# Kernel optimization log

Measured on AMD Instinct MI355X. Metric: run time of the kernel, lower is better.

The kernel has to match this reference:

```python
import jax, jax.numpy as jnp
import numpy as np

N_NODES = 100000
N_EDGES = 1600000
N_GRAPHS = 512
IN_C, HID, OUT_C = 128, 128, 64


def gcn_conv(x, W, b, src, dst, num_nodes):
    # PyG GCNConv: add self-loops, symmetric normalization D^-1/2 (A+I) D^-1/2, then linear.
    h = x @ W  # [N, F_out]
    deg = jnp.ones((num_nodes,), h.dtype).at[dst].add(jnp.ones((src.shape[0],), h.dtype))  # +1 for self-loop
    dinv = jax.lax.rsqrt(deg)
    norm = dinv[src] * dinv[dst]  # [E]
    agg = jnp.zeros_like(h).at[dst].add(h[src] * norm[:, None])
    agg = agg + h * (dinv * dinv)[:, None]  # self-loop contribution
    return agg + b


def global_mean_pool(x, batch, num_graphs):
    s = jax.ops.segment_sum(x, batch, num_segments=num_graphs)
    cnt = jax.ops.segment_sum(jnp.ones((x.shape[0],), x.dtype), batch, num_segments=num_graphs)
    return s / jnp.maximum(cnt, 1.0)[:, None]


def setup_inputs() -> dict:
    key = jax.random.key(0)
    ks = jax.random.split(key, 16)
    glorot = lambda k, i, o: jax.random.normal(k, (i, o), jnp.float32) * (2.0 / (i + o)) ** 0.5
    inp = {
        "x": jax.random.normal(ks[0], (N_NODES, IN_C), jnp.float32),
        "edge_index": jax.random.randint(ks[1], (2, N_EDGES), 0, N_NODES, jnp.int64 if jax.config.jax_enable_x64 else jnp.int32),
        "batch": jnp.sort(jax.random.randint(ks[2], (N_NODES,), 0, N_GRAPHS)),
        "W1": glorot(ks[3], IN_C, HID), "b1": jnp.zeros((HID,), jnp.float32),
        "W2": glorot(ks[4], HID, HID), "b2": jnp.zeros((HID,), jnp.float32),
        "W3": glorot(ks[5], HID, HID), "b3": jnp.zeros((HID,), jnp.float32),
        "Wf1": glorot(ks[6], HID, HID * 4), "bf1": jnp.zeros((HID * 4,), jnp.float32),
        "Wf2": glorot(ks[7], HID * 4, HID * 2), "bf2": jnp.zeros((HID * 2,), jnp.float32),
        "Wf3": glorot(ks[8], HID * 2, HID), "bf3": jnp.zeros((HID,), jnp.float32),
        "Wf4": glorot(ks[9], HID, OUT_C), "bf4": jnp.zeros((OUT_C,), jnp.float32),
    }
    return inp


def reference(x, edge_index, batch, W1, b1, W2, b2, W3, b3,
              Wf1, bf1, Wf2, bf2, Wf3, bf3, Wf4, bf4):
    src, dst = edge_index[0], edge_index[1]
    h = jax.nn.relu(gcn_conv(x, W1, b1, src, dst, N_NODES))
    h = jax.nn.relu(gcn_conv(h, W2, b2, src, dst, N_NODES))
    h = gcn_conv(h, W3, b3, src, dst, N_NODES)
    f = global_mean_pool(h, batch, N_GRAPHS)  # [G, HID]
    z = jax.nn.relu(f @ Wf1 + bf1)
    z = jax.nn.relu(z @ Wf2 + bf2)
    z = jax.nn.relu(z @ Wf3 + bf3)
    z = z @ Wf4 + bf4
    return (f, z)
```

## Files before the change

### kernel.cpp

```cpp
#include <hip/hip_runtime.h>
#include <hip/hip_bf16.h>

#define NN 100000
#define NE 1600000
#define NG 512
#define HID 128
#define PPART 391
#define EPB 4096

typedef __attribute__((ext_vector_type(8))) short short8;
typedef __attribute__((ext_vector_type(4))) float floatx4;

__device__ inline ushort f2bf(float f) {
  uint u = __float_as_uint(f);
  u += 0x7fff + ((u >> 16) & 1);
  return (ushort)(u >> 16);
}
__device__ inline uint pack2(float lo, float hi) {
  return (uint)f2bf(lo) | ((uint)f2bf(hi) << 16);
}
__device__ inline float bflo(uint u) { return __uint_as_float(u << 16); }
__device__ inline float bfhi(uint u) { return __uint_as_float(u & 0xffff0000u); }

__global__ __launch_bounds__(256) void k_hist(const int* __restrict__ dst,
                                              int* __restrict__ phist) {
  __shared__ int h[PPART];
  int t = threadIdx.x;
  for (int i = t; i < PPART; i += 256) h[i] = 0;
  __syncthreads();
  int e0 = blockIdx.x * EPB;
#pragma unroll
  for (int l = 0; l < 16; ++l) {
    int e = e0 + l * 256 + t;
    if (e < NE) atomicAdd(&h[dst[e] >> 8], 1);
  }
  __syncthreads();
  for (int i = t; i < PPART; i += 256)
    if (h[i]) atomicAdd(&phist[i], h[i]);
}

__global__ __launch_bounds__(512) void k_pscan(const int* __restrict__ phist,
                                               int* __restrict__ pbase) {
  __shared__ int ws[8];
  int t = threadIdx.x, lane = t & 63, wid = t >> 6;
  int v = (t < PPART) ? phist[t] : 0;
  int iv = v;
  for (int o = 1; o < 64; o <<= 1) {
    int n = __shfl_up(iv, o, 64);
    if (lane >= o) iv += n;
  }
  if (lane == 63) ws[wid] = iv;
  __syncthreads();
  int add = 0;
#pragma unroll
  for (int w = 0; w < 8; ++w) add += (w < wid) ? ws[w] : 0;
  if (t < PPART) pbase[t] = iv - v + add;
  if (t == 0) {
    int tot = 0;
#pragma unroll
    for (int w = 0; w < 8; ++w) tot += ws[w];
    pbase[PPART] = tot;
  }
}

__global__ void k_pinit(const int* __restrict__ pbase, int* __restrict__ pcur) {
  int p = blockIdx.x * 256 + threadIdx.x;
  if (p < PPART) pcur[p] = pbase[p];
}

__global__ __launch_bounds__(256) void k_part(const int* __restrict__ src,
                                              const int* __restrict__ dst,
                                              int* __restrict__ pcur,
                                              uint* __restrict__ pedge) {
  __shared__ int hist[PPART];
  __shared__ int base[PPART];
  int t = threadIdx.x;
  for (int i = t; i < PPART; i += 256) hist[i] = 0;
  __syncthreads();
  int e0 = blockIdx.x * EPB;
  int d_[16];
#pragma unroll
  for (int l = 0; l < 16; ++l) {
    int e = e0 + l * 256 + t;
    if (e < NE) {
      int d = dst[e];
      d_[l] = d;
      atomicAdd(&hist[d >> 8], 1);
    } else {
      d_[l] = -1;
    }
  }
  __syncthreads();
  for (int i = t; i < PPART; i += 256) {
    int h = hist[i];
    base[i] = h ? atomicAdd(&pcur[i], h) : 0;
  }
  __syncthreads();
#pragma unroll
  for (int l = 0; l < 16; ++l) {
    int e = e0 + l * 256 + t;
    if (e < NE) {
      int d = d_[l];
      int s = src[e];
      int pos = atomicAdd(&base[d >> 8], 1);
      pedge[pos] = (uint)s | ((uint)(d & 255) << 24);
    }
  }
}

__global__ __launch_bounds__(256) void k_bucket2(const int* __restrict__ pbase,
                                                 const uint* __restrict__ pedge,
                                                 int* __restrict__ srcs,
                                                 int* __restrict__ offsets,
                                                 float* __restrict__ dinv) {
  __shared__ int cnt_s[256];
  __shared__ int cur[256];
  __shared__ int ws[4];
  int p = blockIdx.x;
  int n0 = p << 8;
  int t = threadIdx.x;
  int lim = NN - n0; if (lim > 256) lim = 256;
  int s = pbase[p], e = pbase[p + 1];
  cnt_s[t] = 0;
  __syncthreads();
  for (int i = s + t; i < e; i += 256) atomicAdd(&cnt_s[pedge[i] >> 24], 1);
  __syncthreads();
  int v = cnt_s[t];
  int lane = t & 63, wid = t >> 6;
  int iv = v;
  for (int o = 1; o < 64; o <<= 1) {
    int n = __shfl_up(iv, o, 64);
    if (lane >= o) iv += n;
  }
  if (lane == 63) ws[wid] = iv;
  __syncthreads();
  int add = 0;
#pragma unroll
  for (int w = 0; w < 4; ++w) add += (w < wid) ? ws[w] : 0;
  int excl = iv - v + add;
  if (t < lim) {
    int o = s + excl;
    offsets[n0 + t] = o;
    cur[t] = o;
    dinv[n0 + t] = 1.0f / sqrtf((float)(v + 1));
  }
  if (p == PPART - 1 && t == 0) offsets[NN] = NE;
  __syncthreads();
  for (int i = s + t; i < e; i += 256) {
    uint pv = pedge[i];
    int pos = atomicAdd(&cur[pv >> 24], 1);
    srcs[pos] = (int)(pv & 0xFFFFFFu);
  }
}

__global__ void k_cast(const float4* __restrict__ x, uint2* __restrict__ xb, int n4) {
  int i = blockIdx.x * 256 + threadIdx.x;
  if (i < n4) {
    float4 v = x[i];
    uint2 o;
    o.x = pack2(v.x, v.y);
    o.y = pack2(v.z, v.w);
    xb[i] = o;
  }
}

__global__ __launch_bounds__(128) void k_prepW(const float* __restrict__ W,
                                               ushort* __restrict__ wt) {
  int c = blockIdx.x;
  int r = threadIdx.x;
  float v = W[r * 128 + c];
  wt[c * 128 + (((r >> 3) ^ (c & 15)) << 3) + (r & 7)] = f2bf(v);
}

__global__ __launch_bounds__(256) void k_gemm(const ushort* __restrict__ Xb,
                                              const ushort* __restrict__ wt,
                                              ushort* __restrict__ Hb) {
  __shared__ ushort sW[128 * 128];
  int t = threadIdx.x;
#pragma unroll
  for (int l = 0; l < 8; ++l) {
    int idx = t + l * 256;
    ((uint4*)sW)[idx] = ((const uint4*)wt)[idx];
  }
  __syncthreads();
  int wid = t >> 6, lane = t & 63;
  int row0 = blockIdx.x * 64 + wid * 16;
  int arow = row0 + (lane & 15);
  if (arow >= NN) arow = NN - 1;
  const ushort* aptr = Xb + (size_t)arow * 128 + ((lane >> 4) * 8);
  floatx4 acc[8];
#pragma unroll
  for (int n = 0; n < 8; ++n) acc[n] = (floatx4)(0.f);
#pragma unroll
  for (int kb = 0; kb < 4; ++kb) {
    short8 a = *(const short8*)(aptr + kb * 32);
    int kslot = kb * 4 + (lane >> 4);
#pragma unroll
    for (int n = 0; n < 8; ++n) {
      int col = n * 16 + (lane & 15);
      const ushort* bp = sW + col * 128 + ((kslot ^ (col & 15)) << 3);
      short8 b = *(const short8*)bp;
      acc[n] = __builtin_amdgcn_mfma_f32_16x16x32_bf16(a, b, acc[n], 0, 0, 0);
    }
  }
  int srow_base = row0 + (lane >> 4) * 4;
#pragma unroll
  for (int r = 0; r < 4; ++r) {
    int grow = srow_base + r;
    if (grow < NN) {
      ushort* out = Hb + (size_t)grow * 128 + (lane & 15);
#pragma unroll
      for (int n = 0; n < 8; ++n) out[n * 16] = f2bf(acc[n][r]);
    }
  }
}

__global__ __launch_bounds__(256) void k_agg(const ushort* __restrict__ H,
                                             const float* __restrict__ bias,
                                             const float* __restrict__ dinv,
                                             const int* __restrict__ offsets,
                                             const int* __restrict__ srcs,
                                             ushort* __restrict__ Hout, int do_relu) {
  int node = blockIdx.x * 16 + (threadIdx.x >> 4);
  if (node >= NN) return;
  int c8 = threadIdx.x & 15;
  float di = dinv[node];
  int s = offsets[node], e = offsets[node + 1];
  float acc[8];
#pragma unroll
  for (int j = 0; j < 8; ++j) acc[j] = 0.f;
  for (int i = s; i < e; i += 8) {
    int sx[8];
    float dx[8];
    uint4 vx[8];
#pragma unroll
    for (int u = 0; u < 8; ++u) {
      int idx = i + u;
      bool vld = idx < e;
      sx[u] = srcs[vld ? idx : s];
      dx[u] = vld ? 1.0f : 0.0f;
    }
#pragma unroll
    for (int u = 0; u < 8; ++u) dx[u] *= dinv[sx[u]];
#pragma unroll
    for (int u = 0; u < 8; ++u) vx[u] = *((const uint4*)(H + (size_t)sx[u] * 128) + c8);
#pragma unroll
    for (int u = 0; u < 8; ++u) {
      acc[0] += bflo(vx[u].x) * dx[u];
      acc[1] += bfhi(vx[u].x) * dx[u];
      acc[2] += bflo(vx[u].y) * dx[u];
      acc[3] += bfhi(vx[u].y) * dx[u];
      acc[4] += bflo(vx[u].z) * dx[u];
      acc[5] += bfhi(vx[u].z) * dx[u];
      acc[6] += bflo(vx[u].w) * dx[u];
      acc[7] += bfhi(vx[u].w) * dx[u];
    }
  }
  uint4 hv = *((const uint4*)(H + (size_t)node * 128) + c8);
  float hb[8] = {bflo(hv.x), bfhi(hv.x), bflo(hv.y), bfhi(hv.y),
                 bflo(hv.z), bfhi(hv.z), bflo(hv.w), bfhi(hv.w)};
  float dii = di * di;
  const float* bp = bias + c8 * 8;
  float r[8];
#pragma unroll
  for (int j = 0; j < 8; ++j) {
    float vv = acc[j] * di + hb[j] * dii + bp[j];
    if (do_relu) vv = fmaxf(vv, 0.f);
    r[j] = vv;
  }
  uint4 o;
  o.x = pack2(r[0], r[1]);
  o.y = pack2(r[2], r[3]);
  o.z = pack2(r[4], r[5]);
  o.w = pack2(r[6], r[7]);
  *((uint4*)(Hout + (size_t)node * 128) + c8) = o;
}

__device__ inline int lower_bound(const int* a, int n, int v) {
  int lo = 0, hi = n;
  while (lo < hi) {
    int m = (lo + hi) >> 1;
    if (a[m] < v) lo = m + 1; else hi = m;
  }
  return lo;
}

__global__ __launch_bounds__(128) void k_pool(const ushort* __restrict__ H,
                                              const int* __restrict__ batch,
                                              float* __restrict__ f) {
  int g = blockIdx.x;
  int c = threadIdx.x;
  int s = lower_bound(batch, NN, g);
  int e = lower_bound(batch, NN, g + 1);
  float acc = 0.f;
#pragma unroll 4
  for (int i = s; i < e; ++i)
    acc += __uint_as_float(((uint)H[(size_t)i * 128 + c]) << 16);
  f[g * 128 + c] = acc / fmaxf((float)(e - s), 1.0f);
}

__global__ __launch_bounds__(256) void k_mgemm(const float* __restrict__ X,
                                               const float* __restrict__ W,
                                               const float* __restrict__ bias,
                                               float* __restrict__ Y,
                                               int M, int K, int N, int do_relu) {
  __shared__ float sA[32][32];
  __shared__ float sB[32][64];
  int t = threadIdx.x;
  int tn = t & 15, tm = t >> 4;
  int m0 = blockIdx.y * 32;
  int n0 = blockIdx.x * 64;
  float acc[2][4];
#pragma unroll
  for (int i = 0; i < 2; ++i)
#pragma unroll
    for (int j = 0; j < 4; ++j) acc[i][j] = 0.f;

  for (int kb = 0; kb < K; kb += 32) {
    {
      int r = t >> 3, kq = t & 7;
      float4 v = *(const float4*)(X + (size_t)(m0 + r) * K + kb + kq * 4);
      sA[kq * 4 + 0][r] = v.x;
      sA[kq * 4 + 1][r] = v.y;
      sA[kq * 4 + 2][r] = v.z;
      sA[kq * 4 + 3][r] = v.w;
    }
#pragma unroll
    for (int l = 0; l < 2; ++l) {
      int idx = t * 2 + l;
      int kr = idx >> 4, nq = idx & 15;
      *(float4*)&sB[kr][nq * 4] = *(const float4*)(W + (size_t)(kb + kr) * N + n0 + nq * 4);
    }
    __syncthreads();
#pragma unroll
    for (int k = 0; k < 32; ++k) {
      float a[2], b[4];
      a[0] = sA[k][tm * 2];
      a[1] = sA[k][tm * 2 + 1];
      *(float4*)b = *(float4*)&sB[k][tn * 4];
#pragma unroll
      for (int i = 0; i < 2; ++i)
#pragma unroll
        for (int j = 0; j < 4; ++j) acc[i][j] += a[i] * b[j];
    }
    __syncthreads();
  }
  float4 bv = *(const float4*)(bias + n0 + tn * 4);
#pragma unroll
  for (int i = 0; i < 2; ++i) {
    float4 o;
    o.x = acc[i][0] + bv.x;
    o.y = acc[i][1] + bv.y;
    o.z = acc[i][2] + bv.z;
    o.w = acc[i][3] + bv.w;
    if (do_relu) {
      o.x = fmaxf(o.x, 0.f);
      o.y = fmaxf(o.y, 0.f);
      o.z = fmaxf(o.z, 0.f);
      o.w = fmaxf(o.w, 0.f);
    }
    *(float4*)(Y + (size_t)(m0 + tm * 2 + i) * N + n0 + tn * 4) = o;
  }
}

extern "C" void kernel_launch(void* const* d_in, const int* in_sizes, int n_in,
                              void* d_out, int out_size, void* d_ws, size_t ws_size,
                              hipStream_t stream) {
  const float* x    = (const float*)d_in[0];
  const int* ei     = (const int*)d_in[1];
  const int* batch  = (const int*)d_in[2];
  const float* W1   = (const float*)d_in[3];  const float* b1  = (const float*)d_in[4];
  const float* W2   = (const float*)d_in[5];  const float* b2  = (const float*)d_in[6];
  const float* W3   = (const float*)d_in[7];  const float* b3  = (const float*)d_in[8];
  const float* Wf1  = (const float*)d_in[9];  const float* bf1 = (const float*)d_in[10];
  const float* Wf2  = (const float*)d_in[11]; const float* bf2 = (const float*)d_in[12];
  const float* Wf3  = (const float*)d_in[13]; const float* bf3 = (const float*)d_in[14];
  const float* Wf4  = (const float*)d_in[15]; const float* bf4 = (const float*)d_in[16];
  const int* src = ei;
  const int* dst = ei + NE;

  char* ws = (char*)d_ws;
  size_t off = 0;
  auto alloc = [&](size_t bytes) {
    void* p = ws + off;
    off += (bytes + 255) & ~(size_t)255;
    return p;
  };
  ushort* B0     = (ushort*)alloc((size_t)NN * 128 * 2);
  ushort* B1     = (ushort*)alloc((size_t)NN * 128 * 2);
  ushort* B2     = (ushort*)alloc((size_t)NN * 128 * 2);
  float* dinv    = (float*)alloc((size_t)NN * 4);
  int*   offsets = (int*)alloc((size_t)(NN + 1) * 4);
  int*   srcs    = (int*)alloc((size_t)NE * 4);
  uint*  pedge   = (uint*)alloc((size_t)NE * 4);
  int*   phist   = (int*)alloc((size_t)PPART * 4);
  int*   pbase   = (int*)alloc((size_t)(PPART + 1) * 4);
  int*   pcur    = (int*)alloc((size_t)PPART * 4);
  ushort* wt1    = (ushort*)alloc(128 * 128 * 2);
  ushort* wt2    = (ushort*)alloc(128 * 128 * 2);
  ushort* wt3    = (ushort*)alloc(128 * 128 * 2);
  float* t1      = (float*)alloc((size_t)NG * 512 * 4);
  float* t2      = (float*)alloc((size_t)NG * 256 * 4);
  float* t3      = (float*)alloc((size_t)NG * 128 * 4);

  float* f_out = (float*)d_out;
  float* z_out = (float*)d_out + NG * HID;

  hipMemsetAsync(phist, 0, (size_t)PPART * 4, stream);
  k_hist<<<(NE + EPB - 1) / EPB, 256, 0, stream>>>(dst, phist);
  k_pscan<<<1, 512, 0, stream>>>(phist, pbase);
  k_pinit<<<(PPART + 255) / 256, 256, 0, stream>>>(pbase, pcur);
  k_part<<<(NE + EPB - 1) / EPB, 256, 0, stream>>>(src, dst, pcur, pedge);
  k_bucket2<<<PPART, 256, 0, stream>>>(pbase, pedge, srcs, offsets, dinv);

  k_prepW<<<128, 128, 0, stream>>>(W1, wt1);
  k_prepW<<<128, 128, 0, stream>>>(W2, wt2);
  k_prepW<<<128, 128, 0, stream>>>(W3, wt3);
  k_cast<<<(NN * 128 / 4 + 255) / 256, 256, 0, stream>>>((const float4*)x, (uint2*)B0, NN * 128 / 4);

  int gemm_grid = (NN + 63) / 64;
  int agg_grid = (NN + 15) / 16;

  k_gemm<<<gemm_grid, 256, 0, stream>>>(B0, wt1, B1);
  k_agg<<<agg_grid, 256, 0, stream>>>(B1, b1, dinv, offsets, srcs, B2, 1);
  k_gemm<<<gemm_grid, 256, 0, stream>>>(B2, wt2, B1);
  k_agg<<<agg_grid, 256, 0, stream>>>(B1, b2, dinv, offsets, srcs, B0, 1);
  k_gemm<<<gemm_grid, 256, 0, stream>>>(B0, wt3, B1);
  k_agg<<<agg_grid, 256, 0, stream>>>(B1, b3, dinv, offsets, srcs, B2, 0);

  k_pool<<<NG, 128, 0, stream>>>(B2, batch, f_out);

  k_mgemm<<<dim3(8, 16), 256, 0, stream>>>(f_out, Wf1, bf1, t1, NG, 128, 512, 1);
  k_mgemm<<<dim3(4, 16), 256, 0, stream>>>(t1, Wf2, bf2, t2, NG, 512, 256, 1);
  k_mgemm<<<dim3(2, 16), 256, 0, stream>>>(t2, Wf3, bf3, t3, NG, 256, 128, 1);
  k_mgemm<<<dim3(1, 16), 256, 0, stream>>>(t3, Wf4, bf4, z_out, NG, 128, 64, 0);
}
```

Before: 381.4 us.

## Precompute per-edge (src, dinv) metadata and load it cooperatively via shuffles in aggregation

Adds a kernel that packs each CSR edge's source index and the source's dinv into an int2 array, so aggregation no longer does a dependent gather of dinv per edge. In k_agg, the 16 lanes serving a node each load one edge's metadata and broadcast it with wave shuffles, replacing eight redundant per-lane loads of srcs and dinv. It also folds the pcur initialisation into the scan kernel, removing one launch. In exchange it adds an NE-sized buffer, an extra pass over the edges, and loop padding to multiples of 16 edges.

After: 387.3 us. Within noise of the previous version (+1.5%).

```diff
diff --git a/kernel.cpp b/kernel.cpp
--- a/kernel.cpp
+++ b/kernel.cpp
@@ -40,7 +40,8 @@
 }
 
 __global__ __launch_bounds__(512) void k_pscan(const int* __restrict__ phist,
-                                               int* __restrict__ pbase) {
+                                               int* __restrict__ pbase,
+                                               int* __restrict__ pcur) {
   __shared__ int ws[8];
   int t = threadIdx.x, lane = t & 63, wid = t >> 6;
   int v = (t < PPART) ? phist[t] : 0;
@@ -54,18 +55,17 @@
   int add = 0;
 #pragma unroll
   for (int w = 0; w < 8; ++w) add += (w < wid) ? ws[w] : 0;
-  if (t < PPART) pbase[t] = iv - v + add;
+  if (t < PPART) {
+    int b = iv - v + add;
+    pbase[t] = b;
+    pcur[t] = b;
+  }
   if (t == 0) {
     int tot = 0;
 #pragma unroll
     for (int w = 0; w < 8; ++w) tot += ws[w];
     pbase[PPART] = tot;
   }
-}
-
-__global__ void k_pinit(const int* __restrict__ pbase, int* __restrict__ pcur) {
-  int p = blockIdx.x * 256 + threadIdx.x;
-  if (p < PPART) pcur[p] = pbase[p];
 }
 
 __global__ __launch_bounds__(256) void k_part(const int* __restrict__ src,
@@ -153,6 +153,19 @@
   }
 }
 
+__global__ void k_emeta(const int* __restrict__ srcs,
+                        const float* __restrict__ dinv,
+                        int2* __restrict__ emeta) {
+  int i = blockIdx.x * 256 + threadIdx.x;
+  if (i < NE) {
+    int s = srcs[i];
+    int2 m;
+    m.x = s;
+    m.y = __float_as_int(dinv[s]);
+    emeta[i] = m;
+  }
+}
+
 __global__ void k_cast(const float4* __restrict__ x, uint2* __restrict__ xb, int n4) {
   int i = blockIdx.x * 256 + threadIdx.x;
   if (i < n4) {
@@ -219,41 +232,49 @@
                                              const float* __restrict__ bias,
                                              const float* __restrict__ dinv,
                                              const int* __restrict__ offsets,
-                                             const int* __restrict__ srcs,
+                                             const int2* __restrict__ emeta,
                                              ushort* __restrict__ Hout, int do_relu) {
   int node = blockIdx.x * 16 + (threadIdx.x >> 4);
   if (node >= NN) return;
-  int c8 = threadIdx.x & 15;
+  int lane = threadIdx.x & 63;
+  int c8 = lane & 15;
+  int gbase = lane & 48;
   float di = dinv[node];
   int s = offsets[node], e = offsets[node + 1];
   float acc[8];
 #pragma unroll
   for (int j = 0; j < 8; ++j) acc[j] = 0.f;
-  for (int i = s; i < e; i += 8) {
-    int sx[8];
-    float dx[8];
-    uint4 vx[8];
-#pragma unroll
-    for (int u = 0; u < 8; ++u) {
-      int idx = i + u;
-      bool vld = idx < e;
-      sx[u] = srcs[vld ? idx : s];
-      dx[u] = vld ? 1.0f : 0.0f;
-    }
-#pragma unroll
-    for (int u = 0; u < 8; ++u) dx[u] *= dinv[sx[u]];
-#pragma unroll
-    for (int u = 0; u < 8; ++u) vx[u] = *((const uint4*)(H + (size_t)sx[u] * 128) + c8);
-#pragma unroll
-    for (int u = 0; u < 8; ++u) {
-      acc[0] += bflo(vx[u].x) * dx[u];
-      acc[1] += bfhi(vx[u].x) * dx[u];
-      acc[2] += bflo(vx[u].y) * dx[u];
-      acc[3] += bfhi(vx[u].y) * dx[u];
-      acc[4] += bflo(vx[u].z) * dx[u];
-      acc[5] += bfhi(vx[u].z) * dx[u];
-      acc[6] += bflo(vx[u].w) * dx[u];
-      acc[7] += bfhi(vx[u].w) * dx[u];
+  for (int i = s; i < e; i += 16) {
+    int idx = i + c8;
+    bool vld = idx < e;
+    int2 m = emeta[vld ? idx : s];
+    int msrc = m.x;
+    float mw = vld ? __int_as_float(m.y) : 0.0f;
+#pragma unroll
+    for (int half = 0; half < 2; ++half) {
+      int sxu[8];
+      float wu[8];
+#pragma unroll
+      for (int u = 0; u < 8; ++u) {
+        int sl = gbase + half * 8 + u;
+        sxu[u] = __shfl(msrc, sl, 64);
+        wu[u] = __shfl(mw, sl, 64);
+      }
+      uint4 vx[8];
+#pragma unroll
+      for (int u = 0; u < 8; ++u)
+        vx[u] = *((const uint4*)(H + (size_t)sxu[u] * 128) + c8);
+#pragma unroll
+      for (int u = 0; u < 8; ++u) {
+        acc[0] += bflo(vx[u].x) * wu[u];
+        acc[1] += bfhi(vx[u].x) * wu[u];
+        acc[2] += bflo(vx[u].y) * wu[u];
+        acc[3] += bfhi(vx[u].y) * wu[u];
+        acc[4] += bflo(vx[u].z) * wu[u];
+        acc[5] += bfhi(vx[u].z) * wu[u];
+        acc[6] += bflo(vx[u].w) * wu[u];
+        acc[7] += bfhi(vx[u].w) * wu[u];
+      }
     }
   }
   uint4 hv = *((const uint4*)(H + (size_t)node * 128) + c8);
@@ -393,6 +414,7 @@
   int*   offsets = (int*)alloc((size_t)(NN + 1) * 4);
   int*   srcs    = (int*)alloc((size_t)NE * 4);
   uint*  pedge   = (uint*)alloc((size_t)NE * 4);
+  int2*  emeta   = (int2*)alloc((size_t)NE * 8);
   int*   phist   = (int*)alloc((size_t)PPART * 4);
   int*   pbase   = (int*)alloc((size_t)(PPART + 1) * 4);
   int*   pcur    = (int*)alloc((size_t)PPART * 4);
@@ -408,10 +430,10 @@
 
   hipMemsetAsync(phist, 0, (size_t)PPART * 4, stream);
   k_hist<<<(NE + EPB - 1) / EPB, 256, 0, stream>>>(dst, phist);
-  k_pscan<<<1, 512, 0, stream>>>(phist, pbase);
-  k_pinit<<<(PPART + 255) / 256, 256, 0, stream>>>(pbase, pcur);
+  k_pscan<<<1, 512, 0, stream>>>(phist, pbase, pcur);
   k_part<<<(NE + EPB - 1) / EPB, 256, 0, stream>>>(src, dst, pcur, pedge);
   k_bucket2<<<PPART, 256, 0, stream>>>(pbase, pedge, srcs, offsets, dinv);
+  k_emeta<<<(NE + 255) / 256, 256, 0, stream>>>(srcs, dinv, emeta);
 
   k_prepW<<<128, 128, 0, stream>>>(W1, wt1);
   k_prepW<<<128, 128, 0, stream>>>(W2, wt2);
@@ -422,11 +444,11 @@
   int agg_grid = (NN + 15) / 16;
 
   k_gemm<<<gemm_grid, 256, 0, stream>>>(B0, wt1, B1);
-  k_agg<<<agg_grid, 256, 0, stream>>>(B1, b1, dinv, offsets, srcs, B2, 1);
+  k_agg<<<agg_grid, 256, 0, stream>>>(B1, b1, dinv, offsets, emeta, B2, 1);
   k_gemm<<<gemm_grid, 256, 0, stream>>>(B2, wt2, B1);
-  k_agg<<<agg_grid, 256, 0, stream>>>(B1, b2, dinv, offsets, srcs, B0, 1);
+  k_agg<<<agg_grid, 256, 0, stream>>>(B1, b2, dinv, offsets, emeta, B0, 1);
   k_gemm<<<gemm_grid, 256, 0, stream>>>(B0, wt3, B1);
-  k_agg<<<agg_grid, 256, 0, stream>>>(B1, b3, dinv, offsets, srcs, B2, 0);
+  k_agg<<<agg_grid, 256, 0, stream>>>(B1, b3, dinv, offsets, emeta, B2, 0);
 
   k_pool<<<NG, 128, 0, stream>>>(B2, batch, f_out);
 
```
